# Performance work log

Measured on AMD Instinct MI355X. Metric: run time of the kernel, lower is better.

The kernel has to match this reference:

```python
import jax, jax.numpy as jnp
import numpy as np

BIT_SHIFT = 4
PROJECT = True
DIMS = [4096, 4096, 4096, 4096]
BATCH = 8192


def ternarize(w):
    # Ternary weight quantization {-1,0,+1} with straight-through estimator.
    q = jnp.clip(jnp.round(w), -1.0, 1.0)
    return w + jax.lax.stop_gradient(q - w)


def binarize(x):
    # Binary projection sign(x) with hardtanh straight-through estimator.
    c = jnp.clip(x, -1.0, 1.0)
    return c + jax.lax.stop_gradient(jnp.sign(x) - c)


def tern_bin_layer(x, w):
    # Ternary-weight matmul followed by bit-shift scaling (divide by 2**BIT_SHIFT),
    # then optional binary projection of the activation.
    scale = 1.0 / (1 << BIT_SHIFT)
    y = jnp.matmul(x, ternarize(w)) * scale
    if PROJECT:
        y = binarize(y)
    return y


def setup_inputs() -> dict:
    key = jax.random.key(0)
    ks = jax.random.split(key, 4)
    x = jax.random.normal(ks[0], (BATCH, DIMS[0]), dtype=jnp.float32)
    # Latent float weights; ternarized inside the layer.
    W0 = jax.random.normal(ks[1], (DIMS[0], DIMS[1]), dtype=jnp.float32) * 0.7
    W1 = jax.random.normal(ks[2], (DIMS[1], DIMS[2]), dtype=jnp.float32) * 0.7
    W2 = jax.random.normal(ks[3], (DIMS[2], DIMS[3]), dtype=jnp.float32) * 0.7
    return {"x": x, "W0": W0, "W1": W1, "W2": W2}


def reference(x, W0, W1, W2):
    h = tern_bin_layer(x, W0)
    h = tern_bin_layer(h, W1)
    h = tern_bin_layer(h, W2)
    return h
```

## Files before the change

### kernel.cpp

```cpp
#include <hip/hip_runtime.h>
#include <stdint.h>

#define MDIM 8192
#define KDIM 4096
#define NDIM 4096
#define MAXFLAGS (2 * 1024 * 1024)

typedef int i32x4 __attribute__((ext_vector_type(4)));

#define VMCNT(n) asm volatile("s_waitcnt vmcnt(" #n ")" ::: "memory")
#define LGKMCNT0 asm volatile("s_waitcnt lgkmcnt(0)" ::: "memory")
#define SB0 __builtin_amdgcn_sched_barrier(0)

__device__ __forceinline__ void gl2lds16(const void* g, void* l) {
  __builtin_amdgcn_global_load_lds(
      (const __attribute__((address_space(1))) void*)(uintptr_t)(g),
      (__attribute__((address_space(3))) void*)(uintptr_t)(l), 16, 0, 0);
}

__global__ __launch_bounds__(256) void k_prep(const float* __restrict__ x,
                                              const float* __restrict__ W0,
                                              const float* __restrict__ W1,
                                              const float* __restrict__ W2,
                                              int8_t* __restrict__ Qt0,
                                              int8_t* __restrict__ Qt1,
                                              int8_t* __restrict__ Qt2,
                                              int8_t* __restrict__ dig,
                                              int* __restrict__ cnt) {
  const int bid = blockIdx.x;
  const int tid = threadIdx.x;
  if (bid == 0 && tid == 0) *cnt = 0;
  if (bid < 12288) {
    __shared__ int8_t t[64][68];
    const int wsel = bid >> 12;
    const int r = bid & 4095;
    const int n0 = (r & 63) * 64, k0 = (r >> 6) * 64;
    const float* W = (wsel == 0) ? W0 : (wsel == 1) ? W1 : W2;
    int8_t* Qt = (wsel == 0) ? Qt0 : (wsel == 1) ? Qt1 : Qt2;
    const int c4 = tid & 15, rq = tid >> 4;
#pragma unroll
    for (int i = 0; i < 4; ++i) {
      int row = i * 16 + rq;
      float4 v = *(const float4*)&W[(size_t)(k0 + row) * NDIM + n0 + c4 * 4];
      float f[4] = {v.x, v.y, v.z, v.w};
#pragma unroll
      for (int j = 0; j < 4; ++j) {
        float q = fminf(1.f, fmaxf(-1.f, rintf(f[j])));
        t[row][c4 * 4 + j] = (int8_t)(int)q;
      }
    }
    __syncthreads();
#pragma unroll
    for (int i = 0; i < 4; ++i) {
      int n = i * 16 + rq;
      char4 o;
      o.x = t[c4 * 4 + 0][n];
      o.y = t[c4 * 4 + 1][n];
      o.z = t[c4 * 4 + 2][n];
      o.w = t[c4 * 4 + 3][n];
      *(char4*)&Qt[(size_t)(n0 + n) * KDIM + k0 + c4 * 4] = o;
    }
  } else {
    const size_t P = (size_t)MDIM * KDIM;
    size_t i = ((size_t)(bid - 12288) * 256 + tid) * 4;
    float4 v = *(const float4*)(x + i);
    float f[4] = {v.x, v.y, v.z, v.w};
    int8_t dd[3][4];
#pragma unroll
    for (int j = 0; j < 4; ++j) {
      long long s = __double2ll_rn((double)f[j] * 524288.0);
      int8_t d0 = (int8_t)s; s = (s - d0) >> 8;
      int8_t d1 = (int8_t)s; s = (s - d1) >> 8;
      int8_t d2 = (int8_t)s;
      dd[0][j] = d0; dd[1][j] = d1; dd[2][j] = d2;
    }
#pragma unroll
    for (int p = 0; p < 3; ++p) {
      char4 c4v; c4v.x = dd[p][0]; c4v.y = dd[p][1]; c4v.z = dd[p][2]; c4v.w = dd[p][3];
      *(char4*)(dig + p * P + i) = c4v;
    }
  }
}

__global__ __launch_bounds__(512) void k_gemm_l1(const int8_t* __restrict__ dig,
                                                 const int8_t* __restrict__ Qt,
                                                 int8_t* __restrict__ h,
                                                 int* __restrict__ cnt,
                                                 int2* __restrict__ flags) {
  __shared__ __align__(16) int8_t smem[81920];
  const int tid = threadIdx.x;
  const int w = tid >> 6, l = tid & 63;
  const size_t P = (size_t)MDIM * KDIM;

  const int nwg = gridDim.x;
  const int wg = (blockIdx.x & 7) * (nwg >> 3) + (blockIdx.x >> 3);
  const int NB = NDIM / 128;
  const int mb = wg / NB, nb = wg % NB;

  const int srow_in = l >> 2;
  const int scol = (((l & 3) ^ ((l >> 3) & 3)) << 4);
  const bool wA = (w < 6);
  const int8_t *ga0 = nullptr, *ga1 = nullptr;
  const int8_t *gb0 = nullptr, *gb1 = nullptr, *gb2 = nullptr, *gb3 = nullptr;
  if (wA) {
    int i0 = 2 * w, i1 = 2 * w + 1;
    ga0 = dig + (size_t)(i0 >> 2) * P + (size_t)(mb * 64 + (i0 & 3) * 16 + srow_in) * KDIM + scol;
    ga1 = dig + (size_t)(i1 >> 2) * P + (size_t)(mb * 64 + (i1 & 3) * 16 + srow_in) * KDIM + scol;
  } else {
    int j = (w - 6) * 4;
    gb0 = Qt + (size_t)(nb * 128 + (j + 0) * 16 + srow_in) * KDIM + scol;
    gb1 = Qt + (size_t)(nb * 128 + (j + 1) * 16 + srow_in) * KDIM + scol;
    gb2 = Qt + (size_t)(nb * 128 + (j + 2) * 16 + srow_in) * KDIM + scol;
    gb3 = Qt + (size_t)(nb * 128 + (j + 3) * 16 + srow_in) * KDIM + scol;
  }

  i32x4 acc[3][2][2];
#pragma unroll
  for (int p = 0; p < 3; ++p)
#pragma unroll
    for (int mi = 0; mi < 2; ++mi)
#pragma unroll
      for (int ni = 0; ni < 2; ++ni) acc[p][mi][ni] = (i32x4){0, 0, 0, 0};

  const int wr = (w >> 2) * 32;
  const int wc = (w & 3) * 32;
  const int kg = l >> 4;

  auto stage = [&](int buf, int kk) {
    int8_t* sb = smem + buf * 20480;
    if (wA) {
      int8_t* d0 = sb + (2 * w) * 1024;
      gl2lds16(ga0 + kk, d0);
      gl2lds16(ga1 + kk, d0 + 1024);
    } else {
      int8_t* d0 = sb + 12288 + ((w - 6) * 4) * 1024;
      gl2lds16(gb0 + kk, d0);
      gl2lds16(gb1 + kk, d0 + 1024);
      gl2lds16(gb2 + kk, d0 + 2048);
      gl2lds16(gb3 + kk, d0 + 3072);
    }
  };

  auto compute = [&](int buf) {
    const int8_t* sb = smem + buf * 20480;
    i32x4 b[2];
#pragma unroll
    for (int ni = 0; ni < 2; ++ni) {
      int nr = wc + ni * 16 + (l & 15);
      b[ni] = *(const i32x4*)(sb + 12288 + nr * 64 + ((kg ^ ((nr >> 1) & 3)) << 4));
    }
    __builtin_amdgcn_s_setprio(1);
#pragma unroll
    for (int p = 0; p < 3; ++p)
#pragma unroll
      for (int mi = 0; mi < 2; ++mi) {
        int ar = wr + mi * 16 + (l & 15);
        i32x4 a = *(const i32x4*)(sb + p * 4096 + ar * 64 + ((kg ^ ((ar >> 1) & 3)) << 4));
#pragma unroll
        for (int ni = 0; ni < 2; ++ni)
          acc[p][mi][ni] =
              __builtin_amdgcn_mfma_i32_16x16x64_i8(a, b[ni], acc[p][mi][ni], 0, 0, 0);
      }
    __builtin_amdgcn_s_setprio(0);
  };

  const int NT = KDIM / 64;
  stage(0, 0); stage(1, 64); stage(2, 128);
  if (wA) VMCNT(4); else VMCNT(8);
  SB0;
  __builtin_amdgcn_s_barrier();

  for (int t = 0; t < NT; ++t) {
    if (t + 3 < NT) stage((t + 3) & 3, (t + 3) * 64);
    SB0;
    compute(t & 3);
    if (t == NT - 1) break;
    LGKMCNT0;
    if (t + 3 < NT) {
      if (wA) VMCNT(4); else VMCNT(8);
    } else if (t + 2 < NT) {
      if (wA) VMCNT(2); else VMCNT(4);
    } else {
      VMCNT(0);
    }
    SB0;
    __builtin_amdgcn_s_barrier();
  }

  const int mbase = mb * 64 + wr + ((l >> 4) << 2);
  const int nbase = nb * 128 + wc + (l & 15);
#pragma unroll
  for (int mi = 0; mi < 2; ++mi)
#pragma unroll
    for (int ni = 0; ni < 2; ++ni)
#pragma unroll
      for (int j = 0; j < 4; ++j) {
        int s0 = acc[0][mi][ni][j], s1 = acc[1][mi][ni][j];
        int s2 = acc[2][mi][ni][j];
        double d = ((double)s2 * 256.0 + (double)s1) * 256.0 + (double)s0;
        int sg = (d > 0.0) - (d < 0.0);
        int row = mbase + mi * 16 + j;
        int col = nbase + ni * 16;
        h[(size_t)row * NDIM + col] = (int8_t)sg;
        if (fabs(d) <= 2048.0) {
          int idx = atomicAdd(cnt, 1);
          if (idx < MAXFLAGS) flags[idx] = make_int2(row, col);
        }
      }
}

__global__ __launch_bounds__(256) void k_fixup(const float* __restrict__ x,
                                               const int8_t* __restrict__ Qt,
                                               const int* __restrict__ cnt,
                                               const int2* __restrict__ flags,
                                               int8_t* __restrict__ h) {
  __shared__ double red[256];
  int n = *cnt;
  if (n > MAXFLAGS) n = MAXFLAGS;
  for (int i = blockIdx.x; i < n; i += gridDim.x) {
    int2 rc = flags[i];
    const float* xr = x + (size_t)rc.x * KDIM;
    const int8_t* qr = Qt + (size_t)rc.y * KDIM;
    double s = 0.0;
    for (int k = threadIdx.x; k < KDIM; k += 256)
      s += (double)xr[k] * (double)qr[k];
    red[threadIdx.x] = s;
    __syncthreads();
#pragma unroll
    for (int st = 128; st > 0; st >>= 1) {
      if (threadIdx.x < st) red[threadIdx.x] += red[threadIdx.x + st];
      __syncthreads();
    }
    if (threadIdx.x == 0) {
      double d = red[0];
      h[(size_t)rc.x * NDIM + rc.y] = (int8_t)((d > 0.0) - (d < 0.0));
    }
    __syncthreads();
  }
}

template <int F32OUT>
__global__ __launch_bounds__(512, 2) void k_gemm_bin(const int8_t* __restrict__ A,
                                                     const int8_t* __restrict__ Qt,
                                                     void* __restrict__ outp) {
  __shared__ __align__(16) int8_t smem[131072];
  const int tid = threadIdx.x;
  const int w = tid >> 6, l = tid & 63;

  const int nwg = gridDim.x;
  const int wg = (blockIdx.x & 7) * (nwg >> 3) + (blockIdx.x >> 3);
  const int NB = NDIM / 256;
  const int mb = wg / NB, nb = wg % NB;

  const int srow_in = l >> 2;
  const int scol = (((l & 3) ^ ((l >> 3) & 3)) << 4);
  const int8_t* gA[2];
  const int8_t* gB[2];
#pragma unroll
  for (int s = 0; s < 2; ++s) {
    gA[s] = A + (size_t)(mb * 256 + (2 * w + s) * 16 + srow_in) * KDIM + scol;
    gB[s] = Qt + (size_t)(nb * 256 + (2 * w + s) * 16 + srow_in) * KDIM + scol;
  }

  i32x4 acc[8][4];
#pragma unroll
  for (int mi = 0; mi < 8; ++mi)
#pragma unroll
    for (int ni = 0; ni < 4; ++ni) acc[mi][ni] = (i32x4){0, 0, 0, 0};

  const int wr = (w >> 2) * 128, wc = (w & 3) * 64;
  const int kg = l >> 4;

  auto stage = [&](int buf, int kk) {
    int8_t* sb = smem + buf * 32768;
#pragma unroll
    for (int s = 0; s < 2; ++s) {
      gl2lds16(gA[s] + kk, sb + (2 * w + s) * 1024);
      gl2lds16(gB[s] + kk, sb + 16384 + (2 * w + s) * 1024);
    }
  };

  auto compute = [&](int buf) {
    const int8_t* sb = smem + buf * 32768;
    i32x4 b[4], a[8];
#pragma unroll
    for (int ni = 0; ni < 4; ++ni) {
      int nr = wc + ni * 16 + (l & 15);
      b[ni] = *(const i32x4*)(sb + 16384 + nr * 64 + ((kg ^ ((nr >> 1) & 3)) << 4));
    }
#pragma unroll
    for (int mi = 0; mi < 8; ++mi) {
      int ar = wr + mi * 16 + (l & 15);
      a[mi] = *(const i32x4*)(sb + ar * 64 + ((kg ^ ((ar >> 1) & 3)) << 4));
    }
    __builtin_amdgcn_s_setprio(1);
#pragma unroll
    for (int mi = 0; mi < 8; ++mi)
#pragma unroll
      for (int ni = 0; ni < 4; ++ni)
        acc[mi][ni] =
            __builtin_amdgcn_mfma_i32_16x16x64_i8(a[mi], b[ni], acc[mi][ni], 0, 0, 0);
    __builtin_amdgcn_s_setprio(0);
  };

  const int NT = KDIM / 64;
  stage(0, 0); stage(1, 64); stage(2, 128);
  VMCNT(8);
  SB0;
  __builtin_amdgcn_s_barrier();

  for (int t = 0; t < NT; ++t) {
    if (t + 3 < NT) stage((t + 3) & 3, (t + 3) * 64);
    SB0;
    compute(t & 3);
    if (t == NT - 1) break;
    LGKMCNT0;
    if (t + 3 < NT) {
      VMCNT(8);
    } else if (t + 2 < NT) {
      VMCNT(4);
    } else {
      VMCNT(0);
    }
    SB0;
    __builtin_amdgcn_s_barrier();
  }

  const int mbase = mb * 256 + wr + ((l >> 4) << 2);
  const int nbase = nb * 256 + wc + (l & 15);
#pragma unroll
  for (int mi = 0; mi < 8; ++mi)
#pragma unroll
    for (int ni = 0; ni < 4; ++ni)
#pragma unroll
      for (int j = 0; j < 4; ++j) {
        int s = acc[mi][ni][j];
        int sg = (s > 0) - (s < 0);
        size_t off = (size_t)(mbase + mi * 16 + j) * NDIM + (nbase + ni * 16);
        if (F32OUT)
          ((float*)outp)[off] = (float)sg;
        else
          ((int8_t*)outp)[off] = (int8_t)sg;
      }
}

extern "C" void kernel_launch(void* const* d_in, const int* in_sizes, int n_in,
                              void* d_out, int out_size, void* d_ws, size_t ws_size,
                              hipStream_t stream) {
  (void)in_sizes; (void)n_in; (void)out_size; (void)ws_size;
  const float* x  = (const float*)d_in[0];
  const float* W0 = (const float*)d_in[1];
  const float* W1 = (const float*)d_in[2];
  const float* W2 = (const float*)d_in[3];
  float* out = (float*)d_out;

  const size_t QB = (size_t)KDIM * NDIM;
  const size_t HB = (size_t)MDIM * NDIM;
  int8_t* Qt0 = (int8_t*)d_ws;
  int8_t* Qt1 = Qt0 + QB;
  int8_t* Qt2 = Qt1 + QB;
  int8_t* h0  = Qt2 + QB;
  int8_t* h1  = h0 + HB;

  int8_t* dig = (int8_t*)d_out;
  int2* flags = (int2*)((char*)d_out + 3 * HB);
  int* cnt = (int*)((char*)d_out + 3 * HB + (size_t)MAXFLAGS * 8);

  k_prep<<<45056, 256, 0, stream>>>(x, W0, W1, W2, Qt0, Qt1, Qt2, dig, cnt);
  k_gemm_l1<<<(MDIM / 64) * (NDIM / 128), 512, 0, stream>>>(dig, Qt0, h0, cnt, flags);
  k_fixup<<<512, 256, 0, stream>>>(x, Qt0, cnt, flags, h0);
  k_gemm_bin<0><<<(MDIM / 256) * (NDIM / 256), 512, 0, stream>>>(h0, Qt1, h1);
  k_gemm_bin<1><<<(MDIM / 256) * (NDIM / 256), 512, 0, stream>>>(h1, Qt2, out);
}
```

Baseline: 816.3 us.

## Enlarge layer-1 GEMM tile to 128x128 with K=128 double-buffered staging

The first-layer int8 digit GEMM now uses a 128-row M tile, up from 64, and a 128-wide K step. LDS staging drops from a 4-deep ring of 64-wide K tiles to 2-deep double buffering with an 8-way XOR swizzle. All 8 waves now share the loading evenly, and each wave computes a 64x32 sub-tile, which doubles MFMA reuse of every B fragment and halves the number of barriers. The cost is 128KB of LDS (one workgroup per CU), more accumulator registers, and a shallower prefetch pipeline.

```diff
diff --git a/kernel.cpp b/kernel.cpp
--- a/kernel.cpp
+++ b/kernel.cpp
@@ -87,7 +87,7 @@
                                                  int8_t* __restrict__ h,
                                                  int* __restrict__ cnt,
                                                  int2* __restrict__ flags) {
-  __shared__ __align__(16) int8_t smem[81920];
+  __shared__ __align__(16) int8_t smem[131072];
   const int tid = threadIdx.x;
   const int w = tid >> 6, l = tid & 63;
   const size_t P = (size_t)MDIM * KDIM;
@@ -97,89 +97,85 @@
   const int NB = NDIM / 128;
   const int mb = wg / NB, nb = wg % NB;
 
-  const int srow_in = l >> 2;
-  const int scol = (((l & 3) ^ ((l >> 3) & 3)) << 4);
-  const bool wA = (w < 6);
-  const int8_t *ga0 = nullptr, *ga1 = nullptr;
-  const int8_t *gb0 = nullptr, *gb1 = nullptr, *gb2 = nullptr, *gb3 = nullptr;
-  if (wA) {
-    int i0 = 2 * w, i1 = 2 * w + 1;
-    ga0 = dig + (size_t)(i0 >> 2) * P + (size_t)(mb * 64 + (i0 & 3) * 16 + srow_in) * KDIM + scol;
-    ga1 = dig + (size_t)(i1 >> 2) * P + (size_t)(mb * 64 + (i1 & 3) * 16 + srow_in) * KDIM + scol;
-  } else {
-    int j = (w - 6) * 4;
-    gb0 = Qt + (size_t)(nb * 128 + (j + 0) * 16 + srow_in) * KDIM + scol;
-    gb1 = Qt + (size_t)(nb * 128 + (j + 1) * 16 + srow_in) * KDIM + scol;
-    gb2 = Qt + (size_t)(nb * 128 + (j + 2) * 16 + srow_in) * KDIM + scol;
-    gb3 = Qt + (size_t)(nb * 128 + (j + 3) * 16 + srow_in) * KDIM + scol;
-  }
-
-  i32x4 acc[3][2][2];
+  const int swz16 = ((l & 7) ^ (l >> 3)) << 4;
+  const int8_t* gsrc[8];
+  int doff[8];
+#pragma unroll
+  for (int s = 0; s < 8; ++s) {
+    int c = w + 8 * s;
+    if (c < 48) {
+      int p = c >> 4, rb = c & 15;
+      int row = rb * 8 + (l >> 3);
+      gsrc[s] = dig + (size_t)p * P + (size_t)(mb * 128 + row) * KDIM + swz16;
+      doff[s] = c * 1024 + l * 16;
+    } else {
+      int cb = c - 48;
+      int row = cb * 8 + (l >> 3);
+      gsrc[s] = Qt + (size_t)(nb * 128 + row) * KDIM + swz16;
+      doff[s] = 49152 + cb * 1024 + l * 16;
+    }
+  }
+
+  i32x4 acc[3][4][2];
 #pragma unroll
   for (int p = 0; p < 3; ++p)
 #pragma unroll
-    for (int mi = 0; mi < 2; ++mi)
+    for (int mi = 0; mi < 4; ++mi)
 #pragma unroll
       for (int ni = 0; ni < 2; ++ni) acc[p][mi][ni] = (i32x4){0, 0, 0, 0};
 
-  const int wr = (w >> 2) * 32;
-  const int wc = (w & 3) * 32;
-  const int kg = l >> 4;
+  const int wm = w >> 2, wn = w & 3;
 
   auto stage = [&](int buf, int kk) {
-    int8_t* sb = smem + buf * 20480;
-    if (wA) {
-      int8_t* d0 = sb + (2 * w) * 1024;
-      gl2lds16(ga0 + kk, d0);
-      gl2lds16(ga1 + kk, d0 + 1024);
-    } else {
-      int8_t* d0 = sb + 12288 + ((w - 6) * 4) * 1024;
-      gl2lds16(gb0 + kk, d0);
-      gl2lds16(gb1 + kk, d0 + 1024);
-      gl2lds16(gb2 + kk, d0 + 2048);
-      gl2lds16(gb3 + kk, d0 + 3072);
-    }
+#pragma unroll
+    for (int s = 0; s < 8; ++s) gl2lds16(gsrc[s] + kk, smem + buf * 65536 + doff[s]);
   };
 
   auto compute = [&](int buf) {
-    const int8_t* sb = smem + buf * 20480;
-    i32x4 b[2];
-#pragma unroll
-    for (int ni = 0; ni < 2; ++ni) {
-      int nr = wc + ni * 16 + (l & 15);
-      b[ni] = *(const i32x4*)(sb + 12288 + nr * 64 + ((kg ^ ((nr >> 1) & 3)) << 4));
-    }
-    __builtin_amdgcn_s_setprio(1);
-#pragma unroll
-    for (int p = 0; p < 3; ++p)
-#pragma unroll
-      for (int mi = 0; mi < 2; ++mi) {
-        int ar = wr + mi * 16 + (l & 15);
-        i32x4 a = *(const i32x4*)(sb + p * 4096 + ar * 64 + ((kg ^ ((ar >> 1) & 3)) << 4));
-#pragma unroll
-        for (int ni = 0; ni < 2; ++ni)
-          acc[p][mi][ni] =
-              __builtin_amdgcn_mfma_i32_16x16x64_i8(a, b[ni], acc[p][mi][ni], 0, 0, 0);
-      }
-    __builtin_amdgcn_s_setprio(0);
+    const int8_t* sb = smem + buf * 65536;
+#pragma unroll
+    for (int ki = 0; ki < 2; ++ki) {
+      const int kg = ki * 4 + (l >> 4);
+      i32x4 b[2];
+#pragma unroll
+      for (int ni = 0; ni < 2; ++ni) {
+        int nr = wn * 32 + ni * 16 + (l & 15);
+        b[ni] = *(const i32x4*)(sb + 49152 + nr * 128 + ((kg ^ (nr & 7)) << 4));
+      }
+#pragma unroll
+      for (int p = 0; p < 3; ++p) {
+        i32x4 a[4];
+#pragma unroll
+        for (int mi = 0; mi < 4; ++mi) {
+          int ar = wm * 64 + mi * 16 + (l & 15);
+          a[mi] = *(const i32x4*)(sb + p * 16384 + ar * 128 + ((kg ^ (ar & 7)) << 4));
+        }
+        __builtin_amdgcn_s_setprio(1);
+#pragma unroll
+        for (int mi = 0; mi < 4; ++mi)
+#pragma unroll
+          for (int ni = 0; ni < 2; ++ni)
+            acc[p][mi][ni] =
+                __builtin_amdgcn_mfma_i32_16x16x64_i8(a[mi], b[ni], acc[p][mi][ni], 0, 0, 0);
+        __builtin_amdgcn_s_setprio(0);
+      }
+    }
   };
 
-  const int NT = KDIM / 64;
-  stage(0, 0); stage(1, 64); stage(2, 128);
-  if (wA) VMCNT(4); else VMCNT(8);
+  const int NT = KDIM / 128;
+  stage(0, 0); stage(1, 128);
+  VMCNT(8);
   SB0;
   __builtin_amdgcn_s_barrier();
 
   for (int t = 0; t < NT; ++t) {
-    if (t + 3 < NT) stage((t + 3) & 3, (t + 3) * 64);
-    SB0;
-    compute(t & 3);
+    compute(t & 1);
     if (t == NT - 1) break;
-    LGKMCNT0;
-    if (t + 3 < NT) {
-      if (wA) VMCNT(4); else VMCNT(8);
-    } else if (t + 2 < NT) {
-      if (wA) VMCNT(2); else VMCNT(4);
+    LGKMCNT0; SB0;
+    __builtin_amdgcn_s_barrier();
+    if (t + 2 < NT) {
+      stage(t & 1, (t + 2) * 128);
+      VMCNT(8);
     } else {
       VMCNT(0);
     }
@@ -187,10 +183,10 @@
     __builtin_amdgcn_s_barrier();
   }
 
-  const int mbase = mb * 64 + wr + ((l >> 4) << 2);
-  const int nbase = nb * 128 + wc + (l & 15);
-#pragma unroll
-  for (int mi = 0; mi < 2; ++mi)
+  const int mbase = mb * 128 + wm * 64 + ((l >> 4) << 2);
+  const int nbase = nb * 128 + wn * 32 + (l & 15);
+#pragma unroll
+  for (int mi = 0; mi < 4; ++mi)
 #pragma unroll
     for (int ni = 0; ni < 2; ++ni)
 #pragma unroll
@@ -367,7 +363,7 @@
   int* cnt = (int*)((char*)d_out + 3 * HB + (size_t)MAXFLAGS * 8);
 
   k_prep<<<45056, 256, 0, stream>>>(x, W0, W1, W2, Qt0, Qt1, Qt2, dig, cnt);
-  k_gemm_l1<<<(MDIM / 64) * (NDIM / 128), 512, 0, stream>>>(dig, Qt0, h0, cnt, flags);
+  k_gemm_l1<<<(MDIM / 128) * (NDIM / 128), 512, 0, stream>>>(dig, Qt0, h0, cnt, flags);
   k_fixup<<<512, 256, 0, stream>>>(x, Qt0, cnt, flags, h0);
   k_gemm_bin<0><<<(MDIM / 256) * (NDIM / 256), 512, 0, stream>>>(h0, Qt1, h1);
   k_gemm_bin<1><<<(MDIM / 256) * (NDIM / 256), 512, 0, stream>>>(h1, Qt2, out);
```

Result: no change. 810.6 us (-0.7%).

## Widen layer-1 int8 GEMM tile to 64x256 and vectorize digit prep stores

Applied to the files above, without the earlier changes.

The layer-1 three-digit int8 GEMM tile grows from 64x128 to 64x256 columns. Each A digit fragment is now reused across four B fragments, which halves the number of times the A digit planes are re-read from memory. Staging is redistributed over all 8 waves using a generic slot table, LDS use grows to 112KB for four buffers, and the vmcnt waits are adjusted to match. Separately, the x-to-digit prep now has each thread convert 16 floats and write 16-byte stores instead of 4-byte ones. The trade-off is more accumulator registers and LDS per block, which may lower occupancy.

```diff
diff --git a/kernel.cpp b/kernel.cpp
--- a/kernel.cpp
+++ b/kernel.cpp
@@ -7,6 +7,7 @@
 #define MAXFLAGS (2 * 1024 * 1024)
 
 typedef int i32x4 __attribute__((ext_vector_type(4)));
+typedef int i32x4v __attribute__((ext_vector_type(4)));
 
 #define VMCNT(n) asm volatile("s_waitcnt vmcnt(" #n ")" ::: "memory")
 #define LGKMCNT0 asm volatile("s_waitcnt lgkmcnt(0)" ::: "memory")
@@ -62,23 +63,24 @@
     }
   } else {
     const size_t P = (size_t)MDIM * KDIM;
-    size_t i = ((size_t)(bid - 12288) * 256 + tid) * 4;
-    float4 v = *(const float4*)(x + i);
-    float f[4] = {v.x, v.y, v.z, v.w};
-    int8_t dd[3][4];
-#pragma unroll
-    for (int j = 0; j < 4; ++j) {
-      long long s = __double2ll_rn((double)f[j] * 524288.0);
-      int8_t d0 = (int8_t)s; s = (s - d0) >> 8;
-      int8_t d1 = (int8_t)s; s = (s - d1) >> 8;
-      int8_t d2 = (int8_t)s;
-      dd[0][j] = d0; dd[1][j] = d1; dd[2][j] = d2;
-    }
-#pragma unroll
-    for (int p = 0; p < 3; ++p) {
-      char4 c4v; c4v.x = dd[p][0]; c4v.y = dd[p][1]; c4v.z = dd[p][2]; c4v.w = dd[p][3];
-      *(char4*)(dig + p * P + i) = c4v;
-    }
+    size_t i = ((size_t)(bid - 12288) * 256 + tid) * 16;
+    int8_t ob[3][16];
+#pragma unroll
+    for (int q = 0; q < 4; ++q) {
+      float4 v = *(const float4*)(x + i + q * 4);
+      float f[4] = {v.x, v.y, v.z, v.w};
+#pragma unroll
+      for (int j = 0; j < 4; ++j) {
+        long long s = __double2ll_rn((double)f[j] * 524288.0);
+        int8_t d0 = (int8_t)s; s = (s - d0) >> 8;
+        int8_t d1 = (int8_t)s; s = (s - d1) >> 8;
+        int8_t d2 = (int8_t)s;
+        ob[0][q * 4 + j] = d0; ob[1][q * 4 + j] = d1; ob[2][q * 4 + j] = d2;
+      }
+    }
+#pragma unroll
+    for (int p = 0; p < 3; ++p)
+      *(int4*)(dig + p * P + i) = *(const int4*)ob[p];
   }
 }
 
@@ -87,86 +89,84 @@
                                                  int8_t* __restrict__ h,
                                                  int* __restrict__ cnt,
                                                  int2* __restrict__ flags) {
-  __shared__ __align__(16) int8_t smem[81920];
+  __shared__ __align__(16) int8_t smem[114688];
   const int tid = threadIdx.x;
   const int w = tid >> 6, l = tid & 63;
   const size_t P = (size_t)MDIM * KDIM;
 
   const int nwg = gridDim.x;
   const int wg = (blockIdx.x & 7) * (nwg >> 3) + (blockIdx.x >> 3);
-  const int NB = NDIM / 128;
+  const int NB = NDIM / 256;
   const int mb = wg / NB, nb = wg % NB;
 
   const int srow_in = l >> 2;
   const int scol = (((l & 3) ^ ((l >> 3) & 3)) << 4);
-  const bool wA = (w < 6);
-  const int8_t *ga0 = nullptr, *ga1 = nullptr;
-  const int8_t *gb0 = nullptr, *gb1 = nullptr, *gb2 = nullptr, *gb3 = nullptr;
-  if (wA) {
-    int i0 = 2 * w, i1 = 2 * w + 1;
-    ga0 = dig + (size_t)(i0 >> 2) * P + (size_t)(mb * 64 + (i0 & 3) * 16 + srow_in) * KDIM + scol;
-    ga1 = dig + (size_t)(i1 >> 2) * P + (size_t)(mb * 64 + (i1 & 3) * 16 + srow_in) * KDIM + scol;
-  } else {
-    int j = (w - 6) * 4;
-    gb0 = Qt + (size_t)(nb * 128 + (j + 0) * 16 + srow_in) * KDIM + scol;
-    gb1 = Qt + (size_t)(nb * 128 + (j + 1) * 16 + srow_in) * KDIM + scol;
-    gb2 = Qt + (size_t)(nb * 128 + (j + 2) * 16 + srow_in) * KDIM + scol;
-    gb3 = Qt + (size_t)(nb * 128 + (j + 3) * 16 + srow_in) * KDIM + scol;
-  }
-
-  i32x4 acc[3][2][2];
+  const int8_t* gsrc[4];
+  int doff[4];
+#pragma unroll
+  for (int s = 0; s < 4; ++s) {
+    int c = w + 8 * s;
+    if (c >= 28) { gsrc[s] = nullptr; doff[s] = 0; continue; }
+    if (c < 12) {
+      int p = c >> 2, rb = c & 3;
+      gsrc[s] = dig + (size_t)p * P + (size_t)(mb * 64 + rb * 16 + srow_in) * KDIM + scol;
+      doff[s] = c * 1024 + l * 16;
+    } else {
+      int cb = c - 12;
+      gsrc[s] = Qt + (size_t)(nb * 256 + cb * 16 + srow_in) * KDIM + scol;
+      doff[s] = 12288 + cb * 1024 + l * 16;
+    }
+  }
+
+  i32x4 acc[3][2][4];
 #pragma unroll
   for (int p = 0; p < 3; ++p)
 #pragma unroll
     for (int mi = 0; mi < 2; ++mi)
 #pragma unroll
-      for (int ni = 0; ni < 2; ++ni) acc[p][mi][ni] = (i32x4){0, 0, 0, 0};
-
-  const int wr = (w >> 2) * 32;
-  const int wc = (w & 3) * 32;
+      for (int ni = 0; ni < 4; ++ni) acc[p][mi][ni] = (i32x4){0, 0, 0, 0};
+
+  const int wm = w >> 2, wn = w & 3;
   const int kg = l >> 4;
 
   auto stage = [&](int buf, int kk) {
-    int8_t* sb = smem + buf * 20480;
-    if (wA) {
-      int8_t* d0 = sb + (2 * w) * 1024;
-      gl2lds16(ga0 + kk, d0);
-      gl2lds16(ga1 + kk, d0 + 1024);
-    } else {
-      int8_t* d0 = sb + 12288 + ((w - 6) * 4) * 1024;
-      gl2lds16(gb0 + kk, d0);
-      gl2lds16(gb1 + kk, d0 + 1024);
-      gl2lds16(gb2 + kk, d0 + 2048);
-      gl2lds16(gb3 + kk, d0 + 3072);
+#pragma unroll
+    for (int s = 0; s < 4; ++s) {
+      int c = w + 8 * s;
+      if (c < 28) gl2lds16(gsrc[s] + kk, smem + buf * 28672 + doff[s]);
     }
   };
 
   auto compute = [&](int buf) {
-    const int8_t* sb = smem + buf * 20480;
-    i32x4 b[2];
-#pragma unroll
-    for (int ni = 0; ni < 2; ++ni) {
-      int nr = wc + ni * 16 + (l & 15);
+    const int8_t* sb = smem + buf * 28672;
+    i32x4 b[4];
+#pragma unroll
+    for (int ni = 0; ni < 4; ++ni) {
+      int nr = wn * 64 + ni * 16 + (l & 15);
       b[ni] = *(const i32x4*)(sb + 12288 + nr * 64 + ((kg ^ ((nr >> 1) & 3)) << 4));
     }
     __builtin_amdgcn_s_setprio(1);
 #pragma unroll
-    for (int p = 0; p < 3; ++p)
+    for (int p = 0; p < 3; ++p) {
+      i32x4 a[2];
 #pragma unroll
       for (int mi = 0; mi < 2; ++mi) {
-        int ar = wr + mi * 16 + (l & 15);
-        i32x4 a = *(const i32x4*)(sb + p * 4096 + ar * 64 + ((kg ^ ((ar >> 1) & 3)) << 4));
-#pragma unroll
-        for (int ni = 0; ni < 2; ++ni)
+        int ar = wm * 32 + mi * 16 + (l & 15);
+        a[mi] = *(const i32x4*)(sb + p * 4096 + ar * 64 + ((kg ^ ((ar >> 1) & 3)) << 4));
+      }
+#pragma unroll
+      for (int mi = 0; mi < 2; ++mi)
+#pragma unroll
+        for (int ni = 0; ni < 4; ++ni)
           acc[p][mi][ni] =
-              __builtin_amdgcn_mfma_i32_16x16x64_i8(a, b[ni], acc[p][mi][ni], 0, 0, 0);
-      }
+              __builtin_amdgcn_mfma_i32_16x16x64_i8(a[mi], b[ni], acc[p][mi][ni], 0, 0, 0);
+    }
     __builtin_amdgcn_s_setprio(0);
   };
 
   const int NT = KDIM / 64;
   stage(0, 0); stage(1, 64); stage(2, 128);
-  if (wA) VMCNT(4); else VMCNT(8);
+  if (w < 4) VMCNT(8); else VMCNT(6);
   SB0;
   __builtin_amdgcn_s_barrier();
 
@@ -177,9 +177,9 @@
     if (t == NT - 1) break;
     LGKMCNT0;
     if (t + 3 < NT) {
-      if (wA) VMCNT(4); else VMCNT(8);
+      if (w < 4) VMCNT(8); else VMCNT(6);
     } else if (t + 2 < NT) {
-      if (wA) VMCNT(2); else VMCNT(4);
+      if (w < 4) VMCNT(4); else VMCNT(3);
     } else {
       VMCNT(0);
     }
@@ -187,12 +187,12 @@
     __builtin_amdgcn_s_barrier();
   }
 
-  const int mbase = mb * 64 + wr + ((l >> 4) << 2);
-  const int nbase = nb * 128 + wc + (l & 15);
+  const int mbase = mb * 64 + wm * 32 + ((l >> 4) << 2);
+  const int nbase = nb * 256 + wn * 64 + (l & 15);
 #pragma unroll
   for (int mi = 0; mi < 2; ++mi)
 #pragma unroll
-    for (int ni = 0; ni < 2; ++ni)
+    for (int ni = 0; ni < 4; ++ni)
 #pragma unroll
       for (int j = 0; j < 4; ++j) {
         int s0 = acc[0][mi][ni][j], s1 = acc[1][mi][ni][j];
@@ -366,8 +366,8 @@
   int2* flags = (int2*)((char*)d_out + 3 * HB);
   int* cnt = (int*)((char*)d_out + 3 * HB + (size_t)MAXFLAGS * 8);
 
-  k_prep<<<45056, 256, 0, stream>>>(x, W0, W1, W2, Qt0, Qt1, Qt2, dig, cnt);
-  k_gemm_l1<<<(MDIM / 64) * (NDIM / 128), 512, 0, stream>>>(dig, Qt0, h0, cnt, flags);
+  k_prep<<<20480, 256, 0, stream>>>(x, W0, W1, W2, Qt0, Qt1, Qt2, dig, cnt);
+  k_gemm_l1<<<(MDIM / 64) * (NDIM / 256), 512, 0, stream>>>(dig, Qt0, h0, cnt, flags);
   k_fixup<<<512, 256, 0, stream>>>(x, Qt0, cnt, flags, h0);
   k_gemm_bin<0><<<(MDIM / 256) * (NDIM / 256), 512, 0, stream>>>(h0, Qt1, h1);
   k_gemm_bin<1><<<(MDIM / 256) * (NDIM / 256), 512, 0, stream>>>(h1, Qt2, out);
```

Result: faster. 772.0 us (-5.4%).
